# Performance work log

Measured on AMD Instinct MI355X. Metric: run time of the kernel, lower is better.

The kernel has to match this reference:

```python
import jax, jax.numpy as jnp
import numpy as np

BATCH, N_IN, N_OUT, K = 32768, 256, 256, 8

def setup_inputs() -> dict:
    key = jax.random.key(0)
    k1, k2, k3 = jax.random.split(key, 3)
    x = jax.random.normal(k1, (BATCH, N_IN), dtype=jnp.float32)
    coef_a = jax.random.normal(k2, (N_OUT, N_IN, K), dtype=jnp.float32)
    coef_b = jax.random.normal(k3, (N_OUT, N_IN, K), dtype=jnp.float32)
    return {"x": x, "coef_a": coef_a, "coef_b": coef_b}

def reference(x, coef_a, coef_b):
    # Each edge (j, i) applies a univariate Fourier series to x[:, i]:
    #   f_ji(t) = sum_k a[j,i,k] * cos((k+1) t) + b[j,i,k] * sin((k+1) t)
    # Output: S[b, j] = sum_i f_ji(x[b, i])  (activation = identity)
    freqs = jnp.arange(1, K + 1, dtype=x.dtype)          # [K]
    phase = x[:, :, None] * freqs                        # [batch, n_in, K]
    S = (jnp.einsum('bik,jik->bj', jnp.cos(phase), coef_a)
         + jnp.einsum('bik,jik->bj', jnp.sin(phase), coef_b))
    return S
```

## Files before the change

kernel.cpp:

```cpp
#include <hip/hip_runtime.h>
#include <hip/hip_bf16.h>


#define BM 64
#define NST 32

typedef __attribute__((ext_vector_type(8)))  short short8;
typedef __attribute__((ext_vector_type(16))) float f32x16;

static __device__ __forceinline__ unsigned short f2bf(float f) {
    union { float f; unsigned u; } v; v.f = f;
    unsigned r = v.u + 0x7fff + ((v.u >> 16) & 1);
    return (unsigned short)(r >> 16);
}

__global__ __launch_bounds__(256) void pack_w_kernel(
        const float* __restrict__ ca, const float* __restrict__ cb,
        unsigned short* __restrict__ wt) {
    int idx = blockIdx.x * 256 + threadIdx.x;
    int l  = idx & 63;
    int cg = (idx >> 6) & 7;
    int t  = (idx >> 9) & 7;
    int s  = idx >> 12;
    int h  = t >> 2;
    int i  = s * 8 + (t & 3) * 2 + (l >> 5);
    int j  = cg * 32 + (l & 31);
    const float* src = (h ? cb : ca) + ((size_t)j * 256 + i) * 8;
    float4 v0 = ((const float4*)src)[0];
    float4 v1 = ((const float4*)src)[1];
    alignas(16) unsigned short o[8];
    o[0] = f2bf(v0.x); o[1] = f2bf(v0.y); o[2] = f2bf(v0.z); o[3] = f2bf(v0.w);
    o[4] = f2bf(v1.x); o[5] = f2bf(v1.y); o[6] = f2bf(v1.z); o[7] = f2bf(v1.w);
    *(short8*)(wt + (size_t)idx * 8) = *(short8*)o;
}

template<bool PACKED>
__global__ __launch_bounds__(512, 4) void kan_gemm(
        const float* __restrict__ x,
        const unsigned short* __restrict__ bwt,
        const float* __restrict__ ca, const float* __restrict__ cb,
        float* __restrict__ out) {
    __shared__ __align__(16) char Alds[2][16384];

    const int tid  = threadIdx.x;
    const int l    = tid & 63;
    const int w    = tid >> 6;
    const int bm0  = blockIdx.x * BM;
    const int frow = tid >> 3;
    const int fi   = tid & 7;
    const int fswz = frow & 15;
    const int lrow = l & 31;
    const int lhalf = l >> 5;

    f32x16 acc[2];
#pragma unroll
    for (int m = 0; m < 2; ++m)
#pragma unroll
        for (int r = 0; r < 16; ++r) acc[m][r] = 0.0f;

    auto xload = [&](int s) {
        return x[(size_t)(bm0 + frow) * 256 + (size_t)(s * 8 + fi)];
    };

    auto stageA = [&](int buf, float xv) {
        float s1, c1;
        __sincosf(xv, &s1, &c1);
        __hip_bfloat16 fc[8], fs[8];
        fc[0] = __float2bfloat16(c1); fs[0] = __float2bfloat16(s1);
        const float tc = c1 + c1;
        float cp2 = 1.0f, cp1 = c1, sp2 = 0.0f, sp1 = s1;
#pragma unroll
        for (int k = 1; k < 8; ++k) {
            float cn = tc * cp1 - cp2;
            float sn = tc * sp1 - sp2;
            cp2 = cp1; cp1 = cn; sp2 = sp1; sp1 = sn;
            fc[k] = __float2bfloat16(cn); fs[k] = __float2bfloat16(sn);
        }
        char* base = Alds[buf] + frow * 256;
        *(short8*)(base + ((fi       ^ fswz) * 16)) = *(short8*)fc;
        *(short8*)(base + (((8 + fi) ^ fswz) * 16)) = *(short8*)fs;
    };

    auto loadB = [&](int s, int t) -> short8 {
        if (PACKED) {
            return *(const short8*)(bwt
                + ((size_t)(((s * 8 + t) * 8 + w) * 64 + l)) * 8);
        } else {
            const int h = t >> 2;
            const int i = s * 8 + (t & 3) * 2 + lhalf;
            const int j = w * 32 + lrow;
            const float* src = (h ? cb : ca) + ((size_t)j * 256 + i) * 8;
            float4 v0 = ((const float4*)src)[0];
            float4 v1 = ((const float4*)src)[1];
            alignas(16) unsigned short o[8];
            o[0] = f2bf(v0.x); o[1] = f2bf(v0.y);
            o[2] = f2bf(v0.z); o[3] = f2bf(v0.w);
            o[4] = f2bf(v1.x); o[5] = f2bf(v1.y);
            o[6] = f2bf(v1.z); o[7] = f2bf(v1.w);
            return *(short8*)o;
        }
    };

    float xv = xload(0);
    stageA(0, xv);
    float xn = xload(1);
    __syncthreads();

#pragma unroll 1
    for (int s = 0; s < NST; ++s) {
        const int buf = s & 1;

        short8 b0[4];
#pragma unroll
        for (int t = 0; t < 4; ++t) b0[t] = loadB(s, t);

        if (s + 1 < NST) stageA(buf ^ 1, xn);
        if (s + 2 < NST) xn = xload(s + 2);

        short8 b1[4];
#pragma unroll
        for (int t = 0; t < 4; ++t) b1[t] = loadB(s, 4 + t);

#pragma unroll
        for (int t = 0; t < 8; ++t) {
            const short8 bf = (t < 4) ? b0[t & 3] : b1[t & 3];
#pragma unroll
            for (int m = 0; m < 2; ++m) {
                const int row = m * 32 + lrow;
                const int P = (2 * t + lhalf) ^ (row & 15);
                const short8 af = *(const short8*)(Alds[buf] + row * 256 + P * 16);
                acc[m] = __builtin_amdgcn_mfma_f32_32x32x16_bf16(
                    af, bf, acc[m], 0, 0, 0);
            }
        }
        __syncthreads();
    }

    const int col = w * 32 + lrow;
#pragma unroll
    for (int m = 0; m < 2; ++m)
#pragma unroll
        for (int r = 0; r < 16; ++r) {
            const int row = bm0 + m * 32 + (r & 3) + 8 * (r >> 2) + 4 * lhalf;
            out[(size_t)row * 256 + col] = acc[m][r];
        }
}

extern "C" void kernel_launch(void* const* d_in, const int* in_sizes, int n_in,
                              void* d_out, int out_size, void* d_ws, size_t ws_size,
                              hipStream_t stream) {
    const float* x  = (const float*)d_in[0];
    const float* ca = (const float*)d_in[1];
    const float* cb = (const float*)d_in[2];
    float* out = (float*)d_out;

    const size_t wt_bytes = (size_t)131072 * 16;

    if (ws_size >= wt_bytes) {
        unsigned short* wt = (unsigned short*)d_ws;
        pack_w_kernel<<<512, 256, 0, stream>>>(ca, cb, wt);
        kan_gemm<true><<<512, 512, 0, stream>>>(x, wt, ca, cb, out);
    } else {
        kan_gemm<false><<<512, 512, 0, stream>>>(x, nullptr, ca, cb, out);
    }
}
```

Before: 83.07 us.

## Unroll main loop by two with register double-buffered B fragments and precomputed LDS pointers

```diff
diff --git a/kernel.cpp b/kernel.cpp
--- a/kernel.cpp
+++ b/kernel.cpp
@@ -58,14 +58,20 @@
 #pragma unroll
         for (int r = 0; r < 16; ++r) acc[m][r] = 0.0f;
 
-    auto xload = [&](int s) {
-        return x[(size_t)(bm0 + frow) * 256 + (size_t)(s * 8 + fi)];
-    };
+    const float* xp = x + (size_t)(bm0 + frow) * 256 + fi;
+    char* wp0 = Alds[0] + frow * 256 + ((fi       ^ fswz) * 16);
+    char* wp1 = Alds[0] + frow * 256 + (((8 + fi) ^ fswz) * 16);
+    const char* ap[8];
+#pragma unroll
+    for (int t = 0; t < 8; ++t) {
+        const int P = (2 * t + lhalf) ^ (lrow & 15);
+        ap[t] = (const char*)Alds[0] + lrow * 256 + P * 16;
+    }
 
-    auto stageA = [&](int buf, float xv) {
+    auto stageA = [&](int off, float xv) {
         float s1, c1;
         __sincosf(xv, &s1, &c1);
-        __hip_bfloat16 fc[8], fs[8];
+        alignas(16) __hip_bfloat16 fc[8], fs[8];
         fc[0] = __float2bfloat16(c1); fs[0] = __float2bfloat16(s1);
         const float tc = c1 + c1;
         float cp2 = 1.0f, cp1 = c1, sp2 = 0.0f, sp1 = s1;
@@ -76,63 +82,69 @@
             cp2 = cp1; cp1 = cn; sp2 = sp1; sp1 = sn;
             fc[k] = __float2bfloat16(cn); fs[k] = __float2bfloat16(sn);
         }
-        char* base = Alds[buf] + frow * 256;
-        *(short8*)(base + ((fi       ^ fswz) * 16)) = *(short8*)fc;
-        *(short8*)(base + (((8 + fi) ^ fswz) * 16)) = *(short8*)fs;
+        *(short8*)(wp0 + off) = *(short8*)fc;
+        *(short8*)(wp1 + off) = *(short8*)fs;
     };
 
-    auto loadB = [&](int s, int t) -> short8 {
+    auto loadB_all = [&](short8* dst, int s) {
         if (PACKED) {
-            return *(const short8*)(bwt
-                + ((size_t)(((s * 8 + t) * 8 + w) * 64 + l)) * 8);
+            const short8* bp = (const short8*)bwt;
+#pragma unroll
+            for (int t = 0; t < 8; ++t)
+                dst[t] = bp[(size_t)(((s * 8 + t) * 8 + w) * 64 + l)];
         } else {
-            const int h = t >> 2;
-            const int i = s * 8 + (t & 3) * 2 + lhalf;
-            const int j = w * 32 + lrow;
-            const float* src = (h ? cb : ca) + ((size_t)j * 256 + i) * 8;
-            float4 v0 = ((const float4*)src)[0];
-            float4 v1 = ((const float4*)src)[1];
-            alignas(16) unsigned short o[8];
-            o[0] = f2bf(v0.x); o[1] = f2bf(v0.y);
-            o[2] = f2bf(v0.z); o[3] = f2bf(v0.w);
-            o[4] = f2bf(v1.x); o[5] = f2bf(v1.y);
-            o[6] = f2bf(v1.z); o[7] = f2bf(v1.w);
-            return *(short8*)o;
+#pragma unroll
+            for (int t = 0; t < 8; ++t) {
+                const int h = t >> 2;
+                const int i = s * 8 + (t & 3) * 2 + lhalf;
+                const int j = w * 32 + lrow;
+                const float* src = (h ? cb : ca) + ((size_t)j * 256 + i) * 8;
+                float4 v0 = ((const float4*)src)[0];
+                float4 v1 = ((const float4*)src)[1];
+                alignas(16) unsigned short o[8];
+                o[0] = f2bf(v0.x); o[1] = f2bf(v0.y);
+                o[2] = f2bf(v0.z); o[3] = f2bf(v0.w);
+                o[4] = f2bf(v1.x); o[5] = f2bf(v1.y);
+                o[6] = f2bf(v1.z); o[7] = f2bf(v1.w);
+                dst[t] = *(short8*)o;
+            }
         }
     };
 
-    float xv = xload(0);
-    stageA(0, xv);
-    float xn = xload(1);
+    auto mfma_step = [&](int off, const short8* bc) {
+        __builtin_amdgcn_s_setprio(1);
+#pragma unroll
+        for (int t = 0; t < 8; ++t) {
+            const short8 a0 = *(const short8*)(ap[t] + off);
+            acc[0] = __builtin_amdgcn_mfma_f32_32x32x16_bf16(
+                a0, bc[t], acc[0], 0, 0, 0);
+            const short8 a1 = *(const short8*)(ap[t] + off + 8192);
+            acc[1] = __builtin_amdgcn_mfma_f32_32x32x16_bf16(
+                a1, bc[t], acc[1], 0, 0, 0);
+        }
+        __builtin_amdgcn_s_setprio(0);
+    };
+
+    short8 bA[8], bB[8];
+    loadB_all(bA, 0);
+    stageA(0, xp[0]);
+    float xn = xp[8];
     __syncthreads();
 
 #pragma unroll 1
-    for (int s = 0; s < NST; ++s) {
-        const int buf = s & 1;
+    for (int s = 0; s < NST; s += 2) {
+        loadB_all(bB, s + 1);
+        stageA(16384, xn);
+        if (s + 2 < NST) xn = xp[(size_t)(s + 2) * 8];
+        mfma_step(0, bA);
+        __syncthreads();
 
-        short8 b0[4];
-#pragma unroll
-        for (int t = 0; t < 4; ++t) b0[t] = loadB(s, t);
-
-        if (s + 1 < NST) stageA(buf ^ 1, xn);
-        if (s + 2 < NST) xn = xload(s + 2);
-
-        short8 b1[4];
-#pragma unroll
-        for (int t = 0; t < 4; ++t) b1[t] = loadB(s, 4 + t);
-
-#pragma unroll
-        for (int t = 0; t < 8; ++t) {
-            const short8 bf = (t < 4) ? b0[t & 3] : b1[t & 3];
-#pragma unroll
-            for (int m = 0; m < 2; ++m) {
-                const int row = m * 32 + lrow;
-                const int P = (2 * t + lhalf) ^ (row & 15);
-                const short8 af = *(const short8*)(Alds[buf] + row * 256 + P * 16);
-                acc[m] = __builtin_amdgcn_mfma_f32_32x32x16_bf16(
-                    af, bf, acc[m], 0, 0, 0);
-            }
+        if (s + 2 < NST) {
+            loadB_all(bA, s + 2);
+            stageA(0, xn);
+            if (s + 3 < NST) xn = xp[(size_t)(s + 3) * 8];
         }
+        mfma_step(16384, bB);
         __syncthreads();
     }
 
```

Result: slower. 107.8 us (+29.7%).

## Generate Fourier features in registers per wave and drop LDS staging

Applied to the files above, without the earlier changes.

```diff
diff --git a/kernel.cpp b/kernel.cpp
--- a/kernel.cpp
+++ b/kernel.cpp
@@ -2,7 +2,6 @@
 #include <hip/hip_bf16.h>
 
 
-#define BM 64
 #define NST 32
 
 typedef __attribute__((ext_vector_type(8)))  short short8;
@@ -20,12 +19,9 @@
     int idx = blockIdx.x * 256 + threadIdx.x;
     int l  = idx & 63;
     int cg = (idx >> 6) & 7;
-    int t  = (idx >> 9) & 7;
-    int s  = idx >> 12;
-    int h  = t >> 2;
-    int i  = s * 8 + (t & 3) * 2 + (l >> 5);
+    int st = idx >> 9;
     int j  = cg * 32 + (l & 31);
-    const float* src = (h ? cb : ca) + ((size_t)j * 256 + i) * 8;
+    const float* src = ((l >> 5) ? cb : ca) + ((size_t)j * 256 + st) * 8;
     float4 v0 = ((const float4*)src)[0];
     float4 v1 = ((const float4*)src)[1];
     alignas(16) unsigned short o[8];
@@ -40,56 +36,35 @@
         const unsigned short* __restrict__ bwt,
         const float* __restrict__ ca, const float* __restrict__ cb,
         float* __restrict__ out) {
-    __shared__ __align__(16) char Alds[2][16384];
+    const int tid   = threadIdx.x;
+    const int l     = tid & 63;
+    const int w     = tid >> 6;
+    const int lrow  = l & 31;
+    const int lhalf = l >> 5;
+    const int wm    = w & 3;
+    const int wn    = w >> 2;
+    const int rb    = blockIdx.x >> 1;
+    const int ch    = blockIdx.x & 1;
 
-    const int tid  = threadIdx.x;
-    const int l    = tid & 63;
-    const int w    = tid >> 6;
-    const int bm0  = blockIdx.x * BM;
-    const int frow = tid >> 3;
-    const int fi   = tid & 7;
-    const int fswz = frow & 15;
-    const int lrow = l & 31;
-    const int lhalf = l >> 5;
+    const int row  = rb * 128 + wm * 32 + lrow;
+    const int cg0  = ch * 4 + wn * 2;
 
     f32x16 acc[2];
 #pragma unroll
-    for (int m = 0; m < 2; ++m)
+    for (int n = 0; n < 2; ++n)
 #pragma unroll
-        for (int r = 0; r < 16; ++r) acc[m][r] = 0.0f;
+        for (int r = 0; r < 16; ++r) acc[n][r] = 0.0f;
 
-    auto xload = [&](int s) {
-        return x[(size_t)(bm0 + frow) * 256 + (size_t)(s * 8 + fi)];
-    };
+    const float* xp = x + (size_t)row * 256;
+    const float p2init = lhalf ? 0.0f : 1.0f;
 
-    auto stageA = [&](int buf, float xv) {
-        float s1, c1;
-        __sincosf(xv, &s1, &c1);
-        __hip_bfloat16 fc[8], fs[8];
-        fc[0] = __float2bfloat16(c1); fs[0] = __float2bfloat16(s1);
-        const float tc = c1 + c1;
-        float cp2 = 1.0f, cp1 = c1, sp2 = 0.0f, sp1 = s1;
-#pragma unroll
-        for (int k = 1; k < 8; ++k) {
-            float cn = tc * cp1 - cp2;
-            float sn = tc * sp1 - sp2;
-            cp2 = cp1; cp1 = cn; sp2 = sp1; sp1 = sn;
-            fc[k] = __float2bfloat16(cn); fs[k] = __float2bfloat16(sn);
-        }
-        char* base = Alds[buf] + frow * 256;
-        *(short8*)(base + ((fi       ^ fswz) * 16)) = *(short8*)fc;
-        *(short8*)(base + (((8 + fi) ^ fswz) * 16)) = *(short8*)fs;
-    };
-
-    auto loadB = [&](int s, int t) -> short8 {
+    auto loadB = [&](int s, int t, int cg) -> short8 {
         if (PACKED) {
-            return *(const short8*)(bwt
-                + ((size_t)(((s * 8 + t) * 8 + w) * 64 + l)) * 8);
+            return ((const short8*)bwt)[(size_t)(((s * 8 + t) * 8 + cg) * 64 + l)];
         } else {
-            const int h = t >> 2;
-            const int i = s * 8 + (t & 3) * 2 + lhalf;
-            const int j = w * 32 + lrow;
-            const float* src = (h ? cb : ca) + ((size_t)j * 256 + i) * 8;
+            const int j = cg * 32 + lrow;
+            const int i = s * 8 + t;
+            const float* src = (lhalf ? cb : ca) + ((size_t)j * 256 + i) * 8;
             float4 v0 = ((const float4*)src)[0];
             float4 v1 = ((const float4*)src)[1];
             alignas(16) unsigned short o[8];
@@ -101,48 +76,58 @@
         }
     };
 
-    float xv = xload(0);
-    stageA(0, xv);
-    float xn = xload(1);
-    __syncthreads();
+    short8 bq0[4], bq1[4];
+#pragma unroll
+    for (int j = 0; j < 4; ++j) {
+        bq0[j] = loadB(0, j, cg0);
+        bq1[j] = loadB(0, j, cg0 + 1);
+    }
+    float4 xa = *(const float4*)(xp + 0);
+    float4 xb = *(const float4*)(xp + 4);
 
 #pragma unroll 1
     for (int s = 0; s < NST; ++s) {
-        const int buf = s & 1;
-
-        short8 b0[4];
-#pragma unroll
-        for (int t = 0; t < 4; ++t) b0[t] = loadB(s, t);
-
-        if (s + 1 < NST) stageA(buf ^ 1, xn);
-        if (s + 2 < NST) xn = xload(s + 2);
-
-        short8 b1[4];
-#pragma unroll
-        for (int t = 0; t < 4; ++t) b1[t] = loadB(s, 4 + t);
-
 #pragma unroll
         for (int t = 0; t < 8; ++t) {
-            const short8 bf = (t < 4) ? b0[t & 3] : b1[t & 3];
+            const float xv = (t < 4) ? xa[t] : xb[t - 4];
+            float s1, c1;
+            __sincosf(xv, &s1, &c1);
+            float p1 = lhalf ? s1 : c1;
+            float p2 = p2init;
+            alignas(16) __hip_bfloat16 h[8];
+            h[0] = __float2bfloat16(p1);
+            const float tc = c1 + c1;
 #pragma unroll
-            for (int m = 0; m < 2; ++m) {
-                const int row = m * 32 + lrow;
-                const int P = (2 * t + lhalf) ^ (row & 15);
-                const short8 af = *(const short8*)(Alds[buf] + row * 256 + P * 16);
-                acc[m] = __builtin_amdgcn_mfma_f32_32x32x16_bf16(
-                    af, bf, acc[m], 0, 0, 0);
+            for (int k = 1; k < 8; ++k) {
+                const float pn = tc * p1 - p2;
+                p2 = p1; p1 = pn;
+                h[k] = __float2bfloat16(pn);
             }
+            const short8 af = *(const short8*)h;
+
+            __builtin_amdgcn_s_setprio(1);
+            acc[0] = __builtin_amdgcn_mfma_f32_32x32x16_bf16(
+                af, bq0[t & 3], acc[0], 0, 0, 0);
+            acc[1] = __builtin_amdgcn_mfma_f32_32x32x16_bf16(
+                af, bq1[t & 3], acc[1], 0, 0, 0);
+            __builtin_amdgcn_s_setprio(0);
+
+            const int sn = (t < 4) ? s : ((s + 1) & (NST - 1));
+            const int tn = (t + 4) & 7;
+            bq0[t & 3] = loadB(sn, tn, cg0);
+            bq1[t & 3] = loadB(sn, tn, cg0 + 1);
+            if (t == 3) xa = *(const float4*)(xp + (size_t)((s + 1) & (NST - 1)) * 8);
+            if (t == 7) xb = *(const float4*)(xp + (size_t)((s + 1) & (NST - 1)) * 8 + 4);
         }
-        __syncthreads();
     }
 
-    const int col = w * 32 + lrow;
+    const int colb = ch * 128 + wn * 64;
 #pragma unroll
-    for (int m = 0; m < 2; ++m)
+    for (int n = 0; n < 2; ++n)
 #pragma unroll
         for (int r = 0; r < 16; ++r) {
-            const int row = bm0 + m * 32 + (r & 3) + 8 * (r >> 2) + 4 * lhalf;
-            out[(size_t)row * 256 + col] = acc[m][r];
+            const int orow = rb * 128 + wm * 32 + (r & 3) + 8 * (r >> 2) + 4 * lhalf;
+            out[(size_t)orow * 256 + colb + n * 32 + lrow] = acc[n][r];
         }
 }
 
```

After: 117.7 us. 1.42x slower.
